# Performance work log

Measured on AMD Instinct MI355X. Metric: run time of the kernel, lower is better.

Reference implementation:

```python
import jax, jax.numpy as jnp
import numpy as np

HIDDEN = 512
N_STEPS = 24
BATCH = 64
SEQ = 512
LN_EPS = 1e-5


def setup_inputs() -> dict:
    key = jax.random.key(0)
    ks = jax.random.split(key, 12)
    h = HIDDEN
    s = 0.05
    return {
        "enc_outputs": jax.random.normal(ks[0], (BATCH, SEQ, h), jnp.float32),
        "h_prev": jax.random.normal(ks[1], (1, BATCH, h), jnp.float32),
        # additive attention: score = v^T tanh(W_a [dec; enc] + b_a)
        "attn_We": jax.random.normal(ks[2], (h, h), jnp.float32) * s,   # enc half of W_a
        "attn_Wd": jax.random.normal(ks[3], (h, h), jnp.float32) * s,   # dec half of W_a
        "attn_b": jnp.zeros((h,), jnp.float32),
        "attn_v": jax.random.normal(ks[4], (h,), jnp.float32) * s,
        # GRU (PyTorch layout): W_ih (3h, 2h), W_hh (3h, h), gate order r,z,n
        "W_ih": jax.random.normal(ks[5], (3 * h, 2 * h), jnp.float32) * s,
        "W_hh": jax.random.normal(ks[6], (3 * h, h), jnp.float32) * s,
        "b_ih": jnp.zeros((3 * h,), jnp.float32),
        "b_hh": jnp.zeros((3 * h,), jnp.float32),
        # head: LayerNorm -> Linear(h, h//2) -> ReLU -> Linear(h//2, 1)
        "ln_g": jnp.ones((h,), jnp.float32),
        "ln_b": jnp.zeros((h,), jnp.float32),
        "W1": jax.random.normal(ks[7], (h, h // 2), jnp.float32) * s,
        "b1": jnp.zeros((h // 2,), jnp.float32),
        "W2": jax.random.normal(ks[8], (h // 2, 1), jnp.float32) * s,
        "b2": jnp.zeros((1,), jnp.float32),
    }


def _decode(enc_outputs, h0, attn_We, attn_Wd, attn_b, attn_v,
            W_ih, W_hh, b_ih, b_hh, ln_g, ln_b, W1, b1, W2, b2):
    H = enc_outputs.shape[-1]
    # encoder projection is loop-invariant: precompute once
    enc_proj = jnp.einsum("bse,eh->bsh", enc_outputs, attn_We)  # (B,S,H)

    def step(h, _):
        # h: (B, H) decoder state
        # additive attention
        q = h @ attn_Wd + attn_b                                  # (B,H)
        scores = jnp.einsum("bsh,h->bs", jnp.tanh(enc_proj + q[:, None, :]), attn_v)
        alpha = jax.nn.softmax(scores, axis=-1)                   # (B,S)
        context = jnp.einsum("bs,bsh->bh", alpha, enc_outputs)   # (B,H)
        # GRU cell on [context; state]
        x = jnp.concatenate([context, h], axis=-1)                # (B,2H)
        gi = x @ W_ih.T + b_ih                                    # (B,3H)
        gh = h @ W_hh.T + b_hh                                    # (B,3H)
        ir, iz, inn = jnp.split(gi, 3, axis=-1)
        hr, hz, hn = jnp.split(gh, 3, axis=-1)
        r = jax.nn.sigmoid(ir + hr)
        z = jax.nn.sigmoid(iz + hz)
        n = jnp.tanh(inn + r * hn)
        h_new = (1.0 - z) * n + z * h
        # head: LN -> Linear -> ReLU -> Linear
        mu = jnp.mean(h_new, axis=-1, keepdims=True)
        var = jnp.var(h_new, axis=-1, keepdims=True)
        y = (h_new - mu) * jax.lax.rsqrt(var + LN_EPS) * ln_g + ln_b
        y = jax.nn.relu(y @ W1 + b1)
        p = (y @ W2 + b2)[:, 0]                                   # (B,)
        return h_new, p

    h_final, preds = jax.lax.scan(step, h0, None, length=N_STEPS)
    preds = jnp.transpose(preds, (1, 0))[:, :, None]              # (B, n_steps, 1)
    return preds, h_final[None]                                   # (1,B,H)


def reference(enc_outputs, h_prev, attn_We, attn_Wd, attn_b, attn_v,
              W_ih, W_hh, b_ih, b_hh, ln_g, ln_b, W1, b1, W2, b2):
    return _decode(enc_outputs, h_prev[0], attn_We, attn_Wd, attn_b, attn_v,
                   W_ih, W_hh, b_ih, b_hh, ln_g, ln_b, W1, b1, W2, b2)
```

## Files before the change

### kernel.cpp

```cpp
#include <hip/hip_runtime.h>

typedef unsigned short u16;
typedef __attribute__((ext_vector_type(8))) short short8;
typedef __attribute__((ext_vector_type(4))) short short4v;
typedef __attribute__((ext_vector_type(4))) float f32x4;

#define NSTEP 24

__device__ __forceinline__ float b2f(u16 u){ return __uint_as_float(((unsigned)u)<<16); }
__device__ __forceinline__ u16 f2b(float f){
  unsigned u = __float_as_uint(f);
  u += 0x7fffu + ((u>>16)&1u);
  return (u16)(u>>16);
}
__device__ __forceinline__ float tanh_fast(float x){
  x = fminf(12.f, fmaxf(-12.f, x));
  float e = __expf(2.f*x);
  return __fdividef(e-1.f, e+1.f);
}
__device__ __forceinline__ float sigmoid_fast(float x){
  return __fdividef(1.f, 1.f + __expf(-x));
}

__global__ __launch_bounds__(256) void k_cvt(const float* __restrict__ in, u16* __restrict__ out, int n){
  int i = (blockIdx.x*256 + threadIdx.x)*4;
  if (i >= n) return;
  float4 v = *(const float4*)(in + i);
  short4v o;
  o[0] = (short)f2b(v.x); o[1] = (short)f2b(v.y); o[2] = (short)f2b(v.z); o[3] = (short)f2b(v.w);
  *(short4v*)(out + i) = o;
}

__global__ __launch_bounds__(256) void k_transpose512(const float* __restrict__ in, u16* __restrict__ out){
  __shared__ float tile[32][33];
  int tx = threadIdx.x, ty = threadIdx.y;
  int x = blockIdx.x*32 + tx;
  #pragma unroll
  for (int j=0;j<4;++j){
    int y = blockIdx.y*32 + ty + j*8;
    tile[ty+j*8][tx] = in[y*512 + x];
  }
  __syncthreads();
  int x2 = blockIdx.y*32 + tx;
  #pragma unroll
  for (int j=0;j<4;++j){
    int y2 = blockIdx.x*32 + ty + j*8;
    out[y2*512 + x2] = f2b(tile[tx][ty+j*8]);
  }
}

__global__ __launch_bounds__(256) void k_init(const float* __restrict__ h0, float* __restrict__ hf, u16* __restrict__ xcat){
  int idx = blockIdx.x*256 + threadIdx.x;
  float v = h0[idx];
  hf[idx] = v;
  xcat[(idx>>9)*1024 + 512 + (idx&511)] = f2b(v);
}

__global__ __launch_bounds__(256) void k_encproj(const u16* __restrict__ A, const u16* __restrict__ BT, u16* __restrict__ C){
  int w = threadIdx.x>>6, lane = threadIdx.x&63;
  int m0 = blockIdx.x*128 + (w>>1)*64;
  int n0 = blockIdx.y*128 + (w&1)*64;
  int r16 = lane&15, kof = (lane>>4)<<3;
  const u16* Ap = A + (m0+r16)*512 + kof;
  const u16* Bp = BT + (n0+r16)*512 + kof;
  f32x4 acc[4][4];
  #pragma unroll
  for (int i=0;i<4;++i)
    #pragma unroll
    for (int j=0;j<4;++j) acc[i][j] = (f32x4){0.f,0.f,0.f,0.f};
  for (int k0=0;k0<512;k0+=32){
    short8 a[4], b[4];
    #pragma unroll
    for (int mf=0;mf<4;++mf) a[mf] = *(const short8*)(Ap + mf*16*512 + k0);
    #pragma unroll
    for (int nf=0;nf<4;++nf) b[nf] = *(const short8*)(Bp + nf*16*512 + k0);
    #pragma unroll
    for (int mf=0;mf<4;++mf)
      #pragma unroll
      for (int nf=0;nf<4;++nf)
        acc[mf][nf] = __builtin_amdgcn_mfma_f32_16x16x32_bf16(a[mf], b[nf], acc[mf][nf], 0,0,0);
  }
  int rb = (lane>>4)<<2;
  #pragma unroll
  for (int mf=0;mf<4;++mf)
    #pragma unroll
    for (int nf=0;nf<4;++nf)
      #pragma unroll
      for (int r=0;r<4;++r)
        C[(m0+mf*16+rb+r)*512 + n0+nf*16+r16] = f2b(acc[mf][nf][r]);
}

__device__ __forceinline__ void gemm_bt_core(const u16* A, int lda, const u16* BT, int ldb,
    const float* bias, float* C, int ldc, int K, int widx){
  int lane = threadIdx.x & 63;
  int mt = widx & 3, nt = widx >> 2;
  int m0 = mt<<4, n0 = nt<<6;
  int r16 = lane&15, kof = (lane>>4)<<3;
  const u16* Ap = A + (m0+r16)*lda + kof;
  const u16* Bp = BT + (n0+r16)*ldb + kof;
  f32x4 acc[4];
  #pragma unroll
  for (int i=0;i<4;++i) acc[i] = (f32x4){0.f,0.f,0.f,0.f};
  for (int k0=0;k0<K;k0+=32){
    short8 a = *(const short8*)(Ap + k0);
    #pragma unroll
    for (int nf=0;nf<4;++nf){
      short8 b = *(const short8*)(Bp + nf*16*ldb + k0);
      acc[nf] = __builtin_amdgcn_mfma_f32_16x16x32_bf16(a, b, acc[nf], 0,0,0);
    }
  }
  int rb = (lane>>4)<<2;
  #pragma unroll
  for (int nf=0;nf<4;++nf){
    int col = n0 + nf*16 + r16;
    float bv = bias[col];
    #pragma unroll
    for (int r=0;r<4;++r)
      C[(m0+rb+r)*ldc + col] = acc[nf][r] + bv;
  }
}

__global__ __launch_bounds__(256) void k_gemm_q(const u16* __restrict__ xcat, const u16* __restrict__ WdT,
    const float* __restrict__ ab, float* __restrict__ q){
  int widx = blockIdx.x*4 + (threadIdx.x>>6);
  gemm_bt_core(xcat + 512, 1024, WdT, 512, ab, q, 512, 512, widx);
}

__global__ __launch_bounds__(256) void k_gru_gemm(const u16* __restrict__ xcat,
    const u16* __restrict__ Wih, const float* __restrict__ bih,
    const u16* __restrict__ Whh, const float* __restrict__ bhh,
    float* __restrict__ gi, float* __restrict__ gh){
  int widx = blockIdx.x*4 + (threadIdx.x>>6);
  if (blockIdx.y == 0)
    gemm_bt_core(xcat,       1024, Wih, 1024, bih, gi, 1536, 1024, widx);
  else
    gemm_bt_core(xcat + 512, 1024, Whh,  512, bhh, gh, 1536,  512, widx);
}

__global__ __launch_bounds__(256) void k_score(const u16* __restrict__ ep, const float* __restrict__ q,
    const float* __restrict__ av, float* __restrict__ sc){
  __shared__ float qs[512], vs[512];
  int t = threadIdx.x, b = blockIdx.y;
  qs[t]     = q[b*512 + t];
  qs[t+256] = q[b*512 + 256 + t];
  vs[t]     = av[t];
  vs[t+256] = av[256 + t];
  __syncthreads();
  int w = t>>6, lane = t&63;
  float qv[8], vv[8];
  #pragma unroll
  for (int j=0;j<8;++j){ qv[j] = qs[lane*8+j]; vv[j] = vs[lane*8+j]; }
  int s0 = blockIdx.x*16 + w*4;
  #pragma unroll
  for (int i=0;i<4;++i){
    int s = s0 + i;
    short8 e = *(const short8*)(ep + (b*512+s)*512 + lane*8);
    float acc = 0.f;
    #pragma unroll
    for (int j=0;j<8;++j)
      acc += vv[j]*tanh_fast(b2f((u16)e[j]) + qv[j]);
    #pragma unroll
    for (int off=32; off; off>>=1) acc += __shfl_xor(acc, off);
    if (lane==0) sc[b*512 + s] = acc;
  }
}

__global__ __launch_bounds__(256) void k_softctx(const float* __restrict__ sc, const u16* __restrict__ encB,
    u16* __restrict__ xcat){
  __shared__ float red[256];
  __shared__ float al[512];
  __shared__ float part[4][512];
  int t = threadIdx.x, b = blockIdx.x;
  float s1 = sc[b*512 + t], s2 = sc[b*512 + 256 + t];
  red[t] = fmaxf(s1, s2); __syncthreads();
  for (int off=128; off; off>>=1){ if (t<off) red[t] = fmaxf(red[t], red[t+off]); __syncthreads(); }
  float mx = red[0]; __syncthreads();
  float e1 = __expf(s1-mx), e2 = __expf(s2-mx);
  red[t] = e1+e2; __syncthreads();
  for (int off=128; off; off>>=1){ if (t<off) red[t] += red[t+off]; __syncthreads(); }
  float inv = __fdividef(1.f, red[0]);
  al[t] = e1*inv; al[t+256] = e2*inv;
  __syncthreads();
  int hg = (t&63)*8, sch = t>>6;
  float a8[8];
  #pragma unroll
  for (int j=0;j<8;++j) a8[j] = 0.f;
  const u16* eb = encB + (b*512 + sch*128)*512 + hg;
  const float* alp = al + sch*128;
  for (int s=0;s<128;++s){
    short8 e = *(const short8*)(eb + s*512);
    float a = alp[s];
    #pragma unroll
    for (int j=0;j<8;++j) a8[j] += a*b2f((u16)e[j]);
  }
  #pragma unroll
  for (int j=0;j<8;++j) part[sch][hg+j] = a8[j];
  __syncthreads();
  for (int h=t; h<512; h+=256){
    float v = part[0][h]+part[1][h]+part[2][h]+part[3][h];
    xcat[b*1024 + h] = f2b(v);
  }
}

__global__ __launch_bounds__(256) void k_gates(const float* __restrict__ gi, const float* __restrict__ gh,
    float* __restrict__ hf, u16* __restrict__ xcat, float* __restrict__ out, int writeFinal){
  int idx = blockIdx.x*256 + threadIdx.x;
  int b = idx>>9, n = idx&511;
  int gb = b*1536 + n;
  float ir = gi[gb], iz = gi[gb+512], in_ = gi[gb+1024];
  float hr = gh[gb], hz = gh[gb+512], hn  = gh[gb+1024];
  float r = sigmoid_fast(ir+hr);
  float z = sigmoid_fast(iz+hz);
  float nn = tanh_fast(in_ + r*hn);
  float hp = hf[idx];
  float hnew = (1.f-z)*nn + z*hp;
  hf[idx] = hnew;
  xcat[b*1024 + 512 + n] = f2b(hnew);
  if (writeFinal) out[1536 + idx] = hnew;
}

__global__ __launch_bounds__(256) void k_head(const float* __restrict__ hf,
    const float* __restrict__ lng, const float* __restrict__ lnb,
    const float* __restrict__ W1, const float* __restrict__ b1,
    const float* __restrict__ W2, const float* __restrict__ b2,
    float* __restrict__ out, int step){
  __shared__ float yn[512];
  __shared__ float red[256];
  int t = threadIdx.x, b = blockIdx.x;
  float h1 = hf[b*512+t], h2 = hf[b*512+256+t];
  red[t] = h1+h2; __syncthreads();
  for (int off=128; off; off>>=1){ if (t<off) red[t]+=red[t+off]; __syncthreads(); }
  float mu = red[0]*(1.f/512.f); __syncthreads();
  red[t] = h1*h1+h2*h2; __syncthreads();
  for (int off=128; off; off>>=1){ if (t<off) red[t]+=red[t+off]; __syncthreads(); }
  float var = red[0]*(1.f/512.f) - mu*mu; __syncthreads();
  float rs = rsqrtf(var + 1e-5f);
  yn[t]     = (h1-mu)*rs*lng[t] + lnb[t];
  yn[t+256] = (h2-mu)*rs*lng[t+256] + lnb[t+256];
  __syncthreads();
  float acc = b1[t];
  #pragma unroll 8
  for (int k=0;k<512;++k) acc += yn[k]*W1[k*256+t];
  float y = fmaxf(acc, 0.f);
  red[t] = y*W2[t]; __syncthreads();
  for (int off=128; off; off>>=1){ if (t<off) red[t]+=red[t+off]; __syncthreads(); }
  if (t==0) out[b*24 + step] = red[0] + b2[0];
}

extern "C" void kernel_launch(void* const* d_in, const int* in_sizes, int n_in,
                              void* d_out, int out_size, void* d_ws, size_t ws_size,
                              hipStream_t stream){
  (void)in_sizes; (void)n_in; (void)out_size; (void)ws_size;
  const float* enc = (const float*)d_in[0];
  const float* h0  = (const float*)d_in[1];
  const float* We  = (const float*)d_in[2];
  const float* Wd  = (const float*)d_in[3];
  const float* ab  = (const float*)d_in[4];
  const float* av  = (const float*)d_in[5];
  const float* Wih = (const float*)d_in[6];
  const float* Whh = (const float*)d_in[7];
  const float* bih = (const float*)d_in[8];
  const float* bhh = (const float*)d_in[9];
  const float* lng = (const float*)d_in[10];
  const float* lnb = (const float*)d_in[11];
  const float* W1  = (const float*)d_in[12];
  const float* b1  = (const float*)d_in[13];
  const float* W2  = (const float*)d_in[14];
  const float* b2  = (const float*)d_in[15];
  float* out = (float*)d_out;
  char* ws = (char*)d_ws;
  u16*  ep   = (u16*)(ws + 0);
  u16*  encB = (u16*)(ws + 33554432);
  u16*  WeT  = (u16*)(ws + 67108864);
  u16*  WdT  = (u16*)(ws + 67633152);
  u16*  WihB = (u16*)(ws + 68157440);
  u16*  WhhB = (u16*)(ws + 71303168);
  float* hf  = (float*)(ws + 72876032);
  u16*  xcat = (u16*)(ws + 73007104);
  float* q   = (float*)(ws + 73138176);
  float* sc  = (float*)(ws + 73269248);
  float* gi  = (float*)(ws + 73400320);
  float* gh  = (float*)(ws + 73793536);

  k_cvt<<<16384, 256, 0, stream>>>(enc, encB, 16777216);
  k_cvt<<<1536, 256, 0, stream>>>(Wih, WihB, 1572864);
  k_cvt<<<768, 256, 0, stream>>>(Whh, WhhB, 786432);
  k_transpose512<<<dim3(16,16), dim3(32,8), 0, stream>>>(We, WeT);
  k_transpose512<<<dim3(16,16), dim3(32,8), 0, stream>>>(Wd, WdT);
  k_init<<<128, 256, 0, stream>>>(h0, hf, xcat);
  k_encproj<<<dim3(256,4), 256, 0, stream>>>(encB, WeT, ep);
  for (int t=0; t<NSTEP; ++t){
    k_gemm_q<<<8, 256, 0, stream>>>(xcat, WdT, ab, q);
    k_score<<<dim3(32,64), 256, 0, stream>>>(ep, q, av, sc);
    k_softctx<<<64, 256, 0, stream>>>(sc, encB, xcat);
    k_gru_gemm<<<dim3(24,2), 256, 0, stream>>>(xcat, WihB, bih, WhhB, bhh, gi, gh);
    k_gates<<<128, 256, 0, stream>>>(gi, gh, hf, xcat, out, (t==NSTEP-1) ? 1 : 0);
    k_head<<<64, 256, 0, stream>>>(hf, lng, lnb, W1, b1, W2, b2, out, t);
  }
}
```

Measured before the change: 2.164 ms.

## Fuse decode loop into one persistent kernel with grid-wide barriers

Replaces the per-step chain of six kernel launches with a single persistent kernel of 256 blocks that runs all 24 decode steps, synchronising stages through an atomic-counter grid barrier. The GRU hidden-half GEMMs now run concurrently with softmax/context, and the q projection is computed in the head stage per batch row. This removes the launch overhead and idle gaps of about 144 small launches. The cost is barrier spin time, fewer blocks active in some stages, and reliance on all 256 blocks being co-resident. The barrier counter reuses the WeT buffer after the encoder projection has consumed it.

```diff
diff --git a/kernel.cpp b/kernel.cpp
--- a/kernel.cpp
+++ b/kernel.cpp
@@ -6,6 +6,7 @@
 typedef __attribute__((ext_vector_type(4))) float f32x4;
 
 #define NSTEP 24
+#define NB 256
 
 __device__ __forceinline__ float b2f(u16 u){ return __uint_as_float(((unsigned)u)<<16); }
 __device__ __forceinline__ u16 f2b(float f){
@@ -20,6 +21,19 @@
 }
 __device__ __forceinline__ float sigmoid_fast(float x){
   return __fdividef(1.f, 1.f + __expf(-x));
+}
+
+__device__ __forceinline__ void gbar(unsigned* bar){
+  __syncthreads();
+  if (threadIdx.x == 0){
+    __threadfence();
+    unsigned ticket = __hip_atomic_fetch_add(bar, 1u, __ATOMIC_RELAXED, __HIP_MEMORY_SCOPE_AGENT);
+    unsigned target = (ticket/NB + 1u)*NB;
+    while (__hip_atomic_load(bar, __ATOMIC_RELAXED, __HIP_MEMORY_SCOPE_AGENT) < target)
+      __builtin_amdgcn_s_sleep(2);
+  }
+  __syncthreads();
+  __threadfence();
 }
 
 __global__ __launch_bounds__(256) void k_cvt(const float* __restrict__ in, u16* __restrict__ out, int n){
@@ -90,10 +104,9 @@
         C[(m0+mf*16+rb+r)*512 + n0+nf*16+r16] = f2b(acc[mf][nf][r]);
 }
 
-__device__ __forceinline__ void gemm_bt_core(const u16* A, int lda, const u16* BT, int ldb,
-    const float* bias, float* C, int ldc, int K, int widx){
+__device__ __forceinline__ void gemm_tile(const u16* A, int lda, const u16* BT, int ldb,
+    const float* bias, float* C, int ldc, int K, int mt, int nt, bool accum){
   int lane = threadIdx.x & 63;
-  int mt = widx & 3, nt = widx >> 2;
   int m0 = mt<<4, n0 = nt<<6;
   int r16 = lane&15, kof = (lane>>4)<<3;
   const u16* Ap = A + (m0+r16)*lda + kof;
@@ -113,138 +126,187 @@
   #pragma unroll
   for (int nf=0;nf<4;++nf){
     int col = n0 + nf*16 + r16;
-    float bv = bias[col];
-    #pragma unroll
-    for (int r=0;r<4;++r)
-      C[(m0+rb+r)*ldc + col] = acc[nf][r] + bv;
-  }
-}
-
-__global__ __launch_bounds__(256) void k_gemm_q(const u16* __restrict__ xcat, const u16* __restrict__ WdT,
-    const float* __restrict__ ab, float* __restrict__ q){
-  int widx = blockIdx.x*4 + (threadIdx.x>>6);
-  gemm_bt_core(xcat + 512, 1024, WdT, 512, ab, q, 512, 512, widx);
-}
-
-__global__ __launch_bounds__(256) void k_gru_gemm(const u16* __restrict__ xcat,
-    const u16* __restrict__ Wih, const float* __restrict__ bih,
-    const u16* __restrict__ Whh, const float* __restrict__ bhh,
-    float* __restrict__ gi, float* __restrict__ gh){
-  int widx = blockIdx.x*4 + (threadIdx.x>>6);
-  if (blockIdx.y == 0)
-    gemm_bt_core(xcat,       1024, Wih, 1024, bih, gi, 1536, 1024, widx);
-  else
-    gemm_bt_core(xcat + 512, 1024, Whh,  512, bhh, gh, 1536,  512, widx);
-}
-
-__global__ __launch_bounds__(256) void k_score(const u16* __restrict__ ep, const float* __restrict__ q,
-    const float* __restrict__ av, float* __restrict__ sc){
-  __shared__ float qs[512], vs[512];
-  int t = threadIdx.x, b = blockIdx.y;
-  qs[t]     = q[b*512 + t];
-  qs[t+256] = q[b*512 + 256 + t];
-  vs[t]     = av[t];
-  vs[t+256] = av[256 + t];
-  __syncthreads();
-  int w = t>>6, lane = t&63;
-  float qv[8], vv[8];
-  #pragma unroll
-  for (int j=0;j<8;++j){ qv[j] = qs[lane*8+j]; vv[j] = vs[lane*8+j]; }
-  int s0 = blockIdx.x*16 + w*4;
-  #pragma unroll
-  for (int i=0;i<4;++i){
-    int s = s0 + i;
-    short8 e = *(const short8*)(ep + (b*512+s)*512 + lane*8);
-    float acc = 0.f;
-    #pragma unroll
-    for (int j=0;j<8;++j)
-      acc += vv[j]*tanh_fast(b2f((u16)e[j]) + qv[j]);
-    #pragma unroll
-    for (int off=32; off; off>>=1) acc += __shfl_xor(acc, off);
-    if (lane==0) sc[b*512 + s] = acc;
-  }
-}
-
-__global__ __launch_bounds__(256) void k_softctx(const float* __restrict__ sc, const u16* __restrict__ encB,
-    u16* __restrict__ xcat){
-  __shared__ float red[256];
-  __shared__ float al[512];
-  __shared__ float part[4][512];
-  int t = threadIdx.x, b = blockIdx.x;
-  float s1 = sc[b*512 + t], s2 = sc[b*512 + 256 + t];
-  red[t] = fmaxf(s1, s2); __syncthreads();
-  for (int off=128; off; off>>=1){ if (t<off) red[t] = fmaxf(red[t], red[t+off]); __syncthreads(); }
-  float mx = red[0]; __syncthreads();
-  float e1 = __expf(s1-mx), e2 = __expf(s2-mx);
-  red[t] = e1+e2; __syncthreads();
-  for (int off=128; off; off>>=1){ if (t<off) red[t] += red[t+off]; __syncthreads(); }
-  float inv = __fdividef(1.f, red[0]);
-  al[t] = e1*inv; al[t+256] = e2*inv;
-  __syncthreads();
-  int hg = (t&63)*8, sch = t>>6;
-  float a8[8];
-  #pragma unroll
-  for (int j=0;j<8;++j) a8[j] = 0.f;
-  const u16* eb = encB + (b*512 + sch*128)*512 + hg;
-  const float* alp = al + sch*128;
-  for (int s=0;s<128;++s){
-    short8 e = *(const short8*)(eb + s*512);
-    float a = alp[s];
-    #pragma unroll
-    for (int j=0;j<8;++j) a8[j] += a*b2f((u16)e[j]);
-  }
-  #pragma unroll
-  for (int j=0;j<8;++j) part[sch][hg+j] = a8[j];
-  __syncthreads();
-  for (int h=t; h<512; h+=256){
-    float v = part[0][h]+part[1][h]+part[2][h]+part[3][h];
-    xcat[b*1024 + h] = f2b(v);
-  }
-}
-
-__global__ __launch_bounds__(256) void k_gates(const float* __restrict__ gi, const float* __restrict__ gh,
-    float* __restrict__ hf, u16* __restrict__ xcat, float* __restrict__ out, int writeFinal){
-  int idx = blockIdx.x*256 + threadIdx.x;
-  int b = idx>>9, n = idx&511;
-  int gb = b*1536 + n;
-  float ir = gi[gb], iz = gi[gb+512], in_ = gi[gb+1024];
-  float hr = gh[gb], hz = gh[gb+512], hn  = gh[gb+1024];
-  float r = sigmoid_fast(ir+hr);
-  float z = sigmoid_fast(iz+hz);
-  float nn = tanh_fast(in_ + r*hn);
-  float hp = hf[idx];
-  float hnew = (1.f-z)*nn + z*hp;
-  hf[idx] = hnew;
-  xcat[b*1024 + 512 + n] = f2b(hnew);
-  if (writeFinal) out[1536 + idx] = hnew;
-}
-
-__global__ __launch_bounds__(256) void k_head(const float* __restrict__ hf,
+    float bv = bias ? bias[col] : 0.f;
+    #pragma unroll
+    for (int r=0;r<4;++r){
+      float* p = &C[(m0+rb+r)*ldc + col];
+      float v = acc[nf][r] + bv;
+      if (accum) v += *p;
+      *p = v;
+    }
+  }
+}
+
+__device__ __forceinline__ void q_core(const float* hl, const u16* WdT, const float* ab, float* qrow){
+  int tid = threadIdx.x;
+  #pragma unroll
+  for (int jj=0;jj<2;++jj){
+    int j = tid + jj*256;
+    float acc = ab[j];
+    const u16* wr = WdT + j*512;
+    #pragma unroll 4
+    for (int k0=0;k0<512;k0+=8){
+      short8 wv = *(const short8*)(wr + k0);
+      #pragma unroll
+      for (int i=0;i<8;++i) acc = fmaf(hl[k0+i], b2f((u16)wv[i]), acc);
+    }
+    qrow[j] = acc;
+  }
+}
+
+__global__ __launch_bounds__(256) void k_steps(
+    const u16* __restrict__ ep, const u16* __restrict__ encB,
+    const u16* __restrict__ WdT, const u16* __restrict__ WihB, const u16* __restrict__ WhhB,
+    const float* __restrict__ ab, const float* __restrict__ av,
+    const float* __restrict__ bih, const float* __restrict__ bhh,
     const float* __restrict__ lng, const float* __restrict__ lnb,
     const float* __restrict__ W1, const float* __restrict__ b1,
     const float* __restrict__ W2, const float* __restrict__ b2,
-    float* __restrict__ out, int step){
-  __shared__ float yn[512];
-  __shared__ float red[256];
-  int t = threadIdx.x, b = blockIdx.x;
-  float h1 = hf[b*512+t], h2 = hf[b*512+256+t];
-  red[t] = h1+h2; __syncthreads();
-  for (int off=128; off; off>>=1){ if (t<off) red[t]+=red[t+off]; __syncthreads(); }
-  float mu = red[0]*(1.f/512.f); __syncthreads();
-  red[t] = h1*h1+h2*h2; __syncthreads();
-  for (int off=128; off; off>>=1){ if (t<off) red[t]+=red[t+off]; __syncthreads(); }
-  float var = red[0]*(1.f/512.f) - mu*mu; __syncthreads();
-  float rs = rsqrtf(var + 1e-5f);
-  yn[t]     = (h1-mu)*rs*lng[t] + lnb[t];
-  yn[t+256] = (h2-mu)*rs*lng[t+256] + lnb[t+256];
-  __syncthreads();
-  float acc = b1[t];
-  #pragma unroll 8
-  for (int k=0;k<512;++k) acc += yn[k]*W1[k*256+t];
-  float y = fmaxf(acc, 0.f);
-  red[t] = y*W2[t]; __syncthreads();
-  for (int off=128; off; off>>=1){ if (t<off) red[t]+=red[t+off]; __syncthreads(); }
-  if (t==0) out[b*24 + step] = red[0] + b2[0];
+    float* __restrict__ hf, u16* __restrict__ xcat, float* __restrict__ q,
+    float* __restrict__ sc, float* __restrict__ gi, float* __restrict__ gh,
+    float* __restrict__ out, unsigned* __restrict__ bar)
+{
+  __shared__ float sm[2816];
+  int tid = threadIdx.x, bid = blockIdx.x;
+  int wid = tid>>6, lane = tid&63;
+
+  float vv[8];
+  {
+    float4 v0 = *(const float4*)(av + lane*8);
+    float4 v1 = *(const float4*)(av + lane*8 + 4);
+    vv[0]=v0.x; vv[1]=v0.y; vv[2]=v0.z; vv[3]=v0.w;
+    vv[4]=v1.x; vv[5]=v1.y; vv[6]=v1.z; vv[7]=v1.w;
+  }
+
+  if (bid < 64){
+    float* hl = sm;
+    hl[tid] = hf[bid*512 + tid];
+    hl[tid+256] = hf[bid*512 + 256 + tid];
+    __syncthreads();
+    q_core(hl, WdT, ab, q + bid*512);
+  }
+  gbar(bar);
+
+  for (int t=0; t<NSTEP; ++t){
+    {
+      int b = bid>>2;
+      float qv[8];
+      {
+        float4 q0 = *(const float4*)(q + b*512 + lane*8);
+        float4 q1 = *(const float4*)(q + b*512 + lane*8 + 4);
+        qv[0]=q0.x; qv[1]=q0.y; qv[2]=q0.z; qv[3]=q0.w;
+        qv[4]=q1.x; qv[5]=q1.y; qv[6]=q1.z; qv[7]=q1.w;
+      }
+      int srow0 = (bid&3)*128 + wid*32;
+      const u16* eprow = ep + (b*512 + srow0)*512 + lane*8;
+      #pragma unroll 2
+      for (int i=0;i<32;++i){
+        short8 e = *(const short8*)(eprow + i*512);
+        float acc = 0.f;
+        #pragma unroll
+        for (int j=0;j<8;++j)
+          acc += vv[j]*tanh_fast(b2f((u16)e[j]) + qv[j]);
+        #pragma unroll
+        for (int off=32; off; off>>=1) acc += __shfl_xor(acc, off);
+        if (lane==0) sc[b*512 + srow0 + i] = acc;
+      }
+    }
+    gbar(bar);
+
+    if (bid < 64){
+      float* red = sm;
+      float* al  = sm + 256;
+      float* part= sm + 768;
+      int b = bid;
+      float s1 = sc[b*512 + tid], s2 = sc[b*512 + 256 + tid];
+      red[tid] = fmaxf(s1, s2); __syncthreads();
+      for (int off=128; off; off>>=1){ if (tid<off) red[tid] = fmaxf(red[tid], red[tid+off]); __syncthreads(); }
+      float mx = red[0]; __syncthreads();
+      float e1 = __expf(s1-mx), e2 = __expf(s2-mx);
+      red[tid] = e1+e2; __syncthreads();
+      for (int off=128; off; off>>=1){ if (tid<off) red[tid] += red[tid+off]; __syncthreads(); }
+      float inv = __fdividef(1.f, red[0]);
+      al[tid] = e1*inv; al[tid+256] = e2*inv;
+      __syncthreads();
+      int hg = (tid&63)*8, sch = tid>>6;
+      float a8[8];
+      #pragma unroll
+      for (int j=0;j<8;++j) a8[j] = 0.f;
+      const u16* eb = encB + (b*512 + sch*128)*512 + hg;
+      const float* alp = al + sch*128;
+      for (int s=0;s<128;++s){
+        short8 e = *(const short8*)(eb + s*512);
+        float a = alp[s];
+        #pragma unroll
+        for (int j=0;j<8;++j) a8[j] = fmaf(a, b2f((u16)e[j]), a8[j]);
+      }
+      #pragma unroll
+      for (int j=0;j<8;++j) part[sch*512 + hg+j] = a8[j];
+      __syncthreads();
+      for (int h=tid; h<512; h+=256){
+        float v = part[h] + part[512+h] + part[1024+h] + part[1536+h];
+        xcat[b*1024 + h] = f2b(v);
+      }
+    } else if (bid < 88){
+      int w = (bid-64)*4 + wid;
+      gemm_tile(xcat+512, 1024, WhhB, 512, bhh, gh, 1536, 512, w&3, w>>2, false);
+    } else if (bid < 112){
+      int w = (bid-88)*4 + wid;
+      gemm_tile(xcat+512, 1024, WihB+512, 1024, bih, gi, 1536, 512, w&3, w>>2, false);
+    }
+    gbar(bar);
+
+    if (bid < 24){
+      int w = bid*4 + wid;
+      gemm_tile(xcat, 1024, WihB, 1024, (const float*)0, gi, 1536, 512, w&3, w>>2, true);
+    }
+    gbar(bar);
+
+    if (bid < 64){
+      int b = bid;
+      float* hl  = sm;
+      float* yn  = sm + 512;
+      float* red = sm + 1024;
+      #pragma unroll
+      for (int jj=0;jj<2;++jj){
+        int n = tid + jj*256;
+        int gb = b*1536 + n;
+        float r  = sigmoid_fast(gi[gb]      + gh[gb]);
+        float z  = sigmoid_fast(gi[gb+512]  + gh[gb+512]);
+        float nn = tanh_fast(gi[gb+1024] + r*gh[gb+1024]);
+        float hp = hf[b*512 + n];
+        float hnew = (1.f-z)*nn + z*hp;
+        hf[b*512 + n] = hnew;
+        xcat[b*1024 + 512 + n] = f2b(hnew);
+        hl[n] = hnew;
+        if (t == NSTEP-1) out[1536 + b*512 + n] = hnew;
+      }
+      __syncthreads();
+      float h1 = hl[tid], h2 = hl[tid+256];
+      red[tid] = h1+h2; __syncthreads();
+      for (int off=128; off; off>>=1){ if (tid<off) red[tid]+=red[tid+off]; __syncthreads(); }
+      float mu = red[0]*(1.f/512.f); __syncthreads();
+      red[tid] = h1*h1+h2*h2; __syncthreads();
+      for (int off=128; off; off>>=1){ if (tid<off) red[tid]+=red[tid+off]; __syncthreads(); }
+      float var = red[0]*(1.f/512.f) - mu*mu; __syncthreads();
+      float rs = rsqrtf(var + 1e-5f);
+      yn[tid]     = (h1-mu)*rs*lng[tid] + lnb[tid];
+      yn[tid+256] = (h2-mu)*rs*lng[tid+256] + lnb[tid+256];
+      __syncthreads();
+      float acc = b1[tid];
+      #pragma unroll 8
+      for (int k=0;k<512;++k) acc = fmaf(yn[k], W1[k*256+tid], acc);
+      float y = fmaxf(acc, 0.f);
+      red[tid] = y*W2[tid]; __syncthreads();
+      for (int off=128; off; off>>=1){ if (tid<off) red[tid]+=red[tid+off]; __syncthreads(); }
+      if (tid==0) out[b*24 + t] = red[0] + b2[0];
+      if (t < NSTEP-1){
+        __syncthreads();
+        q_core(hl, WdT, ab, q + b*512);
+      }
+    }
+    gbar(bar);
+  }
 }
 
 extern "C" void kernel_launch(void* const* d_in, const int* in_sizes, int n_in,
@@ -281,6 +343,7 @@
   float* sc  = (float*)(ws + 73269248);
   float* gi  = (float*)(ws + 73400320);
   float* gh  = (float*)(ws + 73793536);
+  unsigned* bar = (unsigned*)WeT;
 
   k_cvt<<<16384, 256, 0, stream>>>(enc, encB, 16777216);
   k_cvt<<<1536, 256, 0, stream>>>(Wih, WihB, 1572864);
@@ -289,12 +352,8 @@
   k_transpose512<<<dim3(16,16), dim3(32,8), 0, stream>>>(Wd, WdT);
   k_init<<<128, 256, 0, stream>>>(h0, hf, xcat);
   k_encproj<<<dim3(256,4), 256, 0, stream>>>(encB, WeT, ep);
-  for (int t=0; t<NSTEP; ++t){
-    k_gemm_q<<<8, 256, 0, stream>>>(xcat, WdT, ab, q);
-    k_score<<<dim3(32,64), 256, 0, stream>>>(ep, q, av, sc);
-    k_softctx<<<64, 256, 0, stream>>>(sc, encB, xcat);
-    k_gru_gemm<<<dim3(24,2), 256, 0, stream>>>(xcat, WihB, bih, WhhB, bhh, gi, gh);
-    k_gates<<<128, 256, 0, stream>>>(gi, gh, hf, xcat, out, (t==NSTEP-1) ? 1 : 0);
-    k_head<<<64, 256, 0, stream>>>(hf, lng, lnb, W1, b1, W2, b2, out, t);
-  }
-}
+  hipMemsetAsync(bar, 0, 64, stream);
+  k_steps<<<NB, 256, 0, stream>>>(ep, encB, WdT, WihB, WhhB, ab, av, bih, bhh,
+                                  lng, lnb, W1, b1, W2, b2,
+                                  hf, xcat, q, sc, gi, gh, out, (unsigned*)bar);
+}
```

Result: slower. 7.907 ms (+265.4%).

## Fuse GRU gates, head, and next-step query projection into one kernel

Applied to the files above, without the earlier changes.

Merges the GRU gate update, the LayerNorm/MLP head and the next step's decoder query projection into a single per-batch kernel, dropping two launches per step. The MFMA-based q GEMM becomes a scalar dot-product loop inside the fused kernel, and a separate k_q0 computes the first step's query. The softmax/context kernel moves to 512 threads, so each wave covers 64 sequence positions and the partial sums come from 8 waves. The trade is fewer launches and fewer global round trips against slower scalar q math on only 64 blocks.

```diff
diff --git a/kernel.cpp b/kernel.cpp
--- a/kernel.cpp
+++ b/kernel.cpp
@@ -120,12 +120,6 @@
   }
 }
 
-__global__ __launch_bounds__(256) void k_gemm_q(const u16* __restrict__ xcat, const u16* __restrict__ WdT,
-    const float* __restrict__ ab, float* __restrict__ q){
-  int widx = blockIdx.x*4 + (threadIdx.x>>6);
-  gemm_bt_core(xcat + 512, 1024, WdT, 512, ab, q, 512, 512, widx);
-}
-
 __global__ __launch_bounds__(256) void k_gru_gemm(const u16* __restrict__ xcat,
     const u16* __restrict__ Wih, const float* __restrict__ bih,
     const u16* __restrict__ Whh, const float* __restrict__ bhh,
@@ -137,6 +131,33 @@
     gemm_bt_core(xcat + 512, 1024, Whh,  512, bhh, gh, 1536,  512, widx);
 }
 
+__device__ __forceinline__ void q_core(const float* hl, const u16* WdT, const float* ab, float* qrow){
+  int tid = threadIdx.x;
+  #pragma unroll
+  for (int jj=0;jj<2;++jj){
+    int j = tid + jj*256;
+    float acc = ab[j];
+    const u16* wr = WdT + j*512;
+    #pragma unroll 4
+    for (int k0=0;k0<512;k0+=8){
+      short8 wv = *(const short8*)(wr + k0);
+      #pragma unroll
+      for (int i=0;i<8;++i) acc = fmaf(hl[k0+i], b2f((u16)wv[i]), acc);
+    }
+    qrow[j] = acc;
+  }
+}
+
+__global__ __launch_bounds__(256) void k_q0(const float* __restrict__ hf, const u16* __restrict__ WdT,
+    const float* __restrict__ ab, float* __restrict__ q){
+  __shared__ float hl[512];
+  int t = threadIdx.x, b = blockIdx.x;
+  hl[t] = hf[b*512 + t];
+  hl[t+256] = hf[b*512 + 256 + t];
+  __syncthreads();
+  q_core(hl, WdT, ab, q + b*512);
+}
+
 __global__ __launch_bounds__(256) void k_score(const u16* __restrict__ ep, const float* __restrict__ q,
     const float* __restrict__ av, float* __restrict__ sc){
   __shared__ float qs[512], vs[512];
@@ -165,86 +186,92 @@
   }
 }
 
-__global__ __launch_bounds__(256) void k_softctx(const float* __restrict__ sc, const u16* __restrict__ encB,
+__global__ __launch_bounds__(512) void k_softctx(const float* __restrict__ sc, const u16* __restrict__ encB,
     u16* __restrict__ xcat){
-  __shared__ float red[256];
+  __shared__ float red[512];
   __shared__ float al[512];
-  __shared__ float part[4][512];
+  __shared__ float part[8][512];
   int t = threadIdx.x, b = blockIdx.x;
-  float s1 = sc[b*512 + t], s2 = sc[b*512 + 256 + t];
-  red[t] = fmaxf(s1, s2); __syncthreads();
-  for (int off=128; off; off>>=1){ if (t<off) red[t] = fmaxf(red[t], red[t+off]); __syncthreads(); }
+  float s1 = sc[b*512 + t];
+  red[t] = s1; __syncthreads();
+  for (int off=256; off; off>>=1){ if (t<off) red[t] = fmaxf(red[t], red[t+off]); __syncthreads(); }
   float mx = red[0]; __syncthreads();
-  float e1 = __expf(s1-mx), e2 = __expf(s2-mx);
-  red[t] = e1+e2; __syncthreads();
-  for (int off=128; off; off>>=1){ if (t<off) red[t] += red[t+off]; __syncthreads(); }
+  float e1 = __expf(s1-mx);
+  red[t] = e1; __syncthreads();
+  for (int off=256; off; off>>=1){ if (t<off) red[t] += red[t+off]; __syncthreads(); }
   float inv = __fdividef(1.f, red[0]);
-  al[t] = e1*inv; al[t+256] = e2*inv;
-  __syncthreads();
-  int hg = (t&63)*8, sch = t>>6;
+  al[t] = e1*inv;
+  __syncthreads();
+  int lane = t&63, w = t>>6;
+  int hg = lane*8;
   float a8[8];
   #pragma unroll
   for (int j=0;j<8;++j) a8[j] = 0.f;
-  const u16* eb = encB + (b*512 + sch*128)*512 + hg;
-  const float* alp = al + sch*128;
-  for (int s=0;s<128;++s){
+  const u16* eb = encB + (b*512 + w*64)*512 + hg;
+  const float* alp = al + w*64;
+  for (int s=0;s<64;++s){
     short8 e = *(const short8*)(eb + s*512);
     float a = alp[s];
     #pragma unroll
-    for (int j=0;j<8;++j) a8[j] += a*b2f((u16)e[j]);
-  }
-  #pragma unroll
-  for (int j=0;j<8;++j) part[sch][hg+j] = a8[j];
-  __syncthreads();
-  for (int h=t; h<512; h+=256){
-    float v = part[0][h]+part[1][h]+part[2][h]+part[3][h];
-    xcat[b*1024 + h] = f2b(v);
-  }
-}
-
-__global__ __launch_bounds__(256) void k_gates(const float* __restrict__ gi, const float* __restrict__ gh,
-    float* __restrict__ hf, u16* __restrict__ xcat, float* __restrict__ out, int writeFinal){
-  int idx = blockIdx.x*256 + threadIdx.x;
-  int b = idx>>9, n = idx&511;
-  int gb = b*1536 + n;
-  float ir = gi[gb], iz = gi[gb+512], in_ = gi[gb+1024];
-  float hr = gh[gb], hz = gh[gb+512], hn  = gh[gb+1024];
-  float r = sigmoid_fast(ir+hr);
-  float z = sigmoid_fast(iz+hz);
-  float nn = tanh_fast(in_ + r*hn);
-  float hp = hf[idx];
-  float hnew = (1.f-z)*nn + z*hp;
-  hf[idx] = hnew;
-  xcat[b*1024 + 512 + n] = f2b(hnew);
-  if (writeFinal) out[1536 + idx] = hnew;
-}
-
-__global__ __launch_bounds__(256) void k_head(const float* __restrict__ hf,
+    for (int j=0;j<8;++j) a8[j] = fmaf(a, b2f((u16)e[j]), a8[j]);
+  }
+  #pragma unroll
+  for (int j=0;j<8;++j) part[w][hg+j] = a8[j];
+  __syncthreads();
+  float v = 0.f;
+  #pragma unroll
+  for (int w2=0;w2<8;++w2) v += part[w2][t];
+  xcat[b*1024 + t] = f2b(v);
+}
+
+__global__ __launch_bounds__(256) void k_fin(const float* __restrict__ gi, const float* __restrict__ gh,
     const float* __restrict__ lng, const float* __restrict__ lnb,
     const float* __restrict__ W1, const float* __restrict__ b1,
     const float* __restrict__ W2, const float* __restrict__ b2,
+    const u16* __restrict__ WdT, const float* __restrict__ ab,
+    float* __restrict__ hf, u16* __restrict__ xcat, float* __restrict__ q,
     float* __restrict__ out, int step){
+  __shared__ float hl[512];
   __shared__ float yn[512];
   __shared__ float red[256];
-  int t = threadIdx.x, b = blockIdx.x;
-  float h1 = hf[b*512+t], h2 = hf[b*512+256+t];
-  red[t] = h1+h2; __syncthreads();
-  for (int off=128; off; off>>=1){ if (t<off) red[t]+=red[t+off]; __syncthreads(); }
+  int tid = threadIdx.x, b = blockIdx.x;
+  #pragma unroll
+  for (int jj=0;jj<2;++jj){
+    int n = tid + jj*256;
+    int gb = b*1536 + n;
+    float r  = sigmoid_fast(gi[gb]      + gh[gb]);
+    float z  = sigmoid_fast(gi[gb+512]  + gh[gb+512]);
+    float nn = tanh_fast(gi[gb+1024] + r*gh[gb+1024]);
+    float hp = hf[b*512 + n];
+    float hnew = (1.f-z)*nn + z*hp;
+    hf[b*512 + n] = hnew;
+    xcat[b*1024 + 512 + n] = f2b(hnew);
+    hl[n] = hnew;
+    if (step == NSTEP-1) out[1536 + b*512 + n] = hnew;
+  }
+  __syncthreads();
+  float h1 = hl[tid], h2 = hl[tid+256];
+  red[tid] = h1+h2; __syncthreads();
+  for (int off=128; off; off>>=1){ if (tid<off) red[tid]+=red[tid+off]; __syncthreads(); }
   float mu = red[0]*(1.f/512.f); __syncthreads();
-  red[t] = h1*h1+h2*h2; __syncthreads();
-  for (int off=128; off; off>>=1){ if (t<off) red[t]+=red[t+off]; __syncthreads(); }
+  red[tid] = h1*h1+h2*h2; __syncthreads();
+  for (int off=128; off; off>>=1){ if (tid<off) red[tid]+=red[tid+off]; __syncthreads(); }
   float var = red[0]*(1.f/512.f) - mu*mu; __syncthreads();
   float rs = rsqrtf(var + 1e-5f);
-  yn[t]     = (h1-mu)*rs*lng[t] + lnb[t];
-  yn[t+256] = (h2-mu)*rs*lng[t+256] + lnb[t+256];
-  __syncthreads();
-  float acc = b1[t];
+  yn[tid]     = (h1-mu)*rs*lng[tid] + lnb[tid];
+  yn[tid+256] = (h2-mu)*rs*lng[tid+256] + lnb[tid+256];
+  __syncthreads();
+  float acc = b1[tid];
   #pragma unroll 8
-  for (int k=0;k<512;++k) acc += yn[k]*W1[k*256+t];
+  for (int k=0;k<512;++k) acc = fmaf(yn[k], W1[k*256+tid], acc);
   float y = fmaxf(acc, 0.f);
-  red[t] = y*W2[t]; __syncthreads();
-  for (int off=128; off; off>>=1){ if (t<off) red[t]+=red[t+off]; __syncthreads(); }
-  if (t==0) out[b*24 + step] = red[0] + b2[0];
+  red[tid] = y*W2[tid]; __syncthreads();
+  for (int off=128; off; off>>=1){ if (tid<off) red[tid]+=red[tid+off]; __syncthreads(); }
+  if (tid==0) out[b*24 + step] = red[0] + b2[0];
+  if (step < NSTEP-1){
+    __syncthreads();
+    q_core(hl, WdT, ab, q + b*512);
+  }
 }
 
 extern "C" void kernel_launch(void* const* d_in, const int* in_sizes, int n_in,
@@ -289,12 +316,12 @@
   k_transpose512<<<dim3(16,16), dim3(32,8), 0, stream>>>(Wd, WdT);
   k_init<<<128, 256, 0, stream>>>(h0, hf, xcat);
   k_encproj<<<dim3(256,4), 256, 0, stream>>>(encB, WeT, ep);
+  k_q0<<<64, 256, 0, stream>>>(hf, WdT, ab, q);
   for (int t=0; t<NSTEP; ++t){
-    k_gemm_q<<<8, 256, 0, stream>>>(xcat, WdT, ab, q);
     k_score<<<dim3(32,64), 256, 0, stream>>>(ep, q, av, sc);
-    k_softctx<<<64, 256, 0, stream>>>(sc, encB, xcat);
+    k_softctx<<<64, 512, 0, stream>>>(sc, encB, xcat);
     k_gru_gemm<<<dim3(24,2), 256, 0, stream>>>(xcat, WihB, bih, WhhB, bhh, gi, gh);
-    k_gates<<<128, 256, 0, stream>>>(gi, gh, hf, xcat, out, (t==NSTEP-1) ? 1 : 0);
-    k_head<<<64, 256, 0, stream>>>(hf, lng, lnb, W1, b1, W2, b2, out, t);
-  }
-}
+    k_fin<<<64, 256, 0, stream>>>(gi, gh, lng, lnb, W1, b1, W2, b2, WdT, ab,
+                                  hf, xcat, q, out, t);
+  }
+}
```

Result: no change. 2.164 ms (-0.0%).
